# Kernel optimization log

Measured on AMD Instinct MI355X. Metric: run time of the kernel, lower is better.

Reference implementation:

```python
import jax, jax.numpy as jnp
import numpy as np

N_SITES = 64   # number of sampled indices (n = 2**6 in source)
CHI = 64       # virtual bond dimension of the isometric TN
BATCH = 32768  # number of independent perfect samples


def _isometrize(W):
    """Right-canonical isometrization (analog of mera.isometrize(method='cayley')).

    W: [n, chi, 2, chi] raw params -> A with sum_{s,r} A[l,s,r] A[l',s,r] = delta_{ll'}.
    """
    n, chi = W.shape[0], W.shape[1]
    M = W.reshape(n, chi, 2 * chi)               # [n, chi, 2*chi]
    Q, _ = jnp.linalg.qr(jnp.swapaxes(M, 1, 2))  # [n, 2*chi, chi], orthonormal columns
    return jnp.swapaxes(Q, 1, 2).reshape(n, chi, 2, chi)


def setup_inputs() -> dict:
    key = jax.random.key(0)
    k1, k2 = jax.random.split(key)
    W = jax.random.normal(k1, (N_SITES, CHI, 2, CHI), dtype=jnp.float32)
    u = jax.random.uniform(k2, (BATCH, N_SITES), dtype=jnp.float32)
    return {"W": W, "u": u}


def reference(W, u):
    """Perfect (autoregressive exact-conditional) sampling from an isometric TN.

    Returns:
      s_hat: [B, n, 2] one-hot samples, outcome 0 -> [0,1], outcome 1 -> [1,0]
             (matching v0=[0,1], v1=[1,0] in the source)
      prob:  [B, n] conditional probability of the drawn outcome at each step
             (the `probability` array the source maintains).
    """
    A = _isometrize(W)                 # [n, chi, 2, chi]
    B, n = u.shape
    chi = W.shape[1]
    # left boundary environment (unit norm) -> total norm is exactly 1
    L0 = jnp.zeros((B, chi), dtype=W.dtype).at[:, 0].set(1.0)

    def step(L, inp):
        A_i, u_i = inp                              # [chi,2,chi], [B]
        T = jnp.einsum('bl,lsr->bsr', L, A_i)       # [B, 2, chi]
        p = jnp.sum(T * T, axis=-1)                 # [B, 2]; p0 + p1 == 1 by isometry
        take1 = u_i >= p[:, 0]                      # r < ps0 -> outcome 0
        s = take1.astype(jnp.int32)
        p_s = jnp.where(take1, p[:, 1], p[:, 0])    # probability of chosen branch
        T_s = jnp.where(take1[:, None], T[:, 1, :], T[:, 0, :])
        L_new = T_s / jnp.sqrt(p_s)[:, None]        # renormalize by sqrt(prob)
        return L_new, (s, p_s)

    _, (s, p) = jax.lax.scan(step, L0, (A, u.T))    # s,p: [n, B]
    s = s.T                                         # [B, n]
    prob = p.T                                      # [B, n]
    s_hat = jax.nn.one_hot(1 - s, 2, dtype=W.dtype)  # 0 -> [0,1], 1 -> [1,0]
    return s_hat, prob
```

## Files before the change

kernel.cpp:

```cpp
#include <hip/hip_runtime.h>

#define NSITES 64
#define CHI 64
#define BATCH 32768
#define LPAD 66

typedef double d4 __attribute__((ext_vector_type(4)));

#define MFMA_HAZARD_FENCE() do {                                    \
    __builtin_amdgcn_sched_barrier(0);                              \
    asm volatile("s_nop 7\n\ts_nop 7\n\ts_nop 7\n\ts_nop 7" :::);   \
    __builtin_amdgcn_sched_barrier(0);                              \
} while (0)

__global__ __launch_bounds__(512) void qr_site_kernel(
    const float* __restrict__ W, double* __restrict__ A8)
{
    __shared__ double M[128][65];
    __shared__ double wpart[8][64];
    __shared__ double tauS[64];
    __shared__ double redS[2];
    __shared__ double vcol[136];

    const int i   = blockIdx.x;
    const int tid = threadIdx.x;

    for (int idx = tid; idx < 8192; idx += 512) {
        int l = idx >> 7, sr = idx & 127;
        M[sr][l] = (double)W[i * 8192 + idx];
    }
    __syncthreads();

    const int jf = tid & 63;
    const int gf = tid >> 6;
    const int r0 = gf * 16;

    for (int k = 0; k < 64; ++k) {
        const double alpha = M[k][k];
        double v2 = 0.0;
        if (tid < 128) { double xv = (tid > k) ? M[tid][k] : 0.0; v2 = xv * xv; }
        #pragma unroll
        for (int off = 32; off; off >>= 1) v2 += __shfl_down(v2, off, 64);
        if (tid < 128 && (tid & 63) == 0) redS[tid >> 6] = v2;
        __syncthreads();
        const double xnorm2 = redS[0] + redS[1];

        double beta, tk;
        if (xnorm2 == 0.0) { beta = alpha; tk = 0.0; }
        else {
            double nrm = sqrt(alpha * alpha + xnorm2);
            beta = (alpha >= 0.0) ? -nrm : nrm;
            tk   = (beta - alpha) / beta;
        }
        const double sc = (tk != 0.0) ? (1.0 / (alpha - beta)) : 0.0;
        if (tid < 128 && tid > k && tk != 0.0) M[tid][k] *= sc;
        if (tid == 0) tauS[k] = tk;
        __syncthreads();

        double part = 0.0;
        if (jf > k) {
            #pragma unroll 4
            for (int m = 0; m < 16; ++m) {
                int rr = r0 + m;
                double vr = (rr > k) ? M[rr][k] : ((rr == k) ? 1.0 : 0.0);
                part = fma(vr, M[rr][jf], part);
            }
        }
        wpart[gf][jf] = part;
        __syncthreads();
        if (jf > k) {
            double wj = tauS[k] * (wpart[0][jf] + wpart[1][jf] + wpart[2][jf] + wpart[3][jf]
                                 + wpart[4][jf] + wpart[5][jf] + wpart[6][jf] + wpart[7][jf]);
            #pragma unroll 4
            for (int m = 0; m < 16; ++m) {
                int rr = r0 + m;
                double vr = (rr > k) ? M[rr][k] : ((rr == k) ? 1.0 : 0.0);
                M[rr][jf] = fma(-vr, wj, M[rr][jf]);
            }
        }
        __syncthreads();
    }

    const int jq = tid >> 3;
    const int qq = tid & 7;
    double E[16];
    #pragma unroll
    for (int m = 0; m < 16; ++m) E[m] = ((qq * 16 + m) == jq) ? 1.0 : 0.0;

    for (int k = 63; k >= 0; --k) {
        if (tid < 128) {
            double val = (tid > k) ? M[tid][k] : ((tid == k) ? 1.0 : 0.0);
            vcol[tid + (tid >> 4)] = val;
        }
        __syncthreads();
        const double tk = tauS[k];
        double part = 0.0;
        #pragma unroll
        for (int m = 0; m < 16; ++m) {
            int rr = qq * 16 + m;
            part = fma(vcol[rr + qq], E[m], part);
        }
        part += __shfl_xor(part, 1, 64);
        part += __shfl_xor(part, 2, 64);
        part += __shfl_xor(part, 4, 64);
        const double wj = tk * part;
        #pragma unroll
        for (int m = 0; m < 16; ++m) {
            int rr = qq * 16 + m;
            E[m] = fma(-vcol[rr + qq], wj, E[m]);
        }
        __syncthreads();
    }

    double* dst = A8 + (size_t)i * 8192 + jq * 128 + qq * 16;
    #pragma unroll
    for (int m = 0; m < 16; ++m) dst[m] = E[m];
}

#define MFMA_ROW(bp, a)                                                   \
    c0 = __builtin_amdgcn_mfma_f64_16x16x4f64((a), (bp)[  0], c0, 0,0,0); \
    c1 = __builtin_amdgcn_mfma_f64_16x16x4f64((a), (bp)[ 16], c1, 0,0,0); \
    c2 = __builtin_amdgcn_mfma_f64_16x16x4f64((a), (bp)[ 32], c2, 0,0,0); \
    c3 = __builtin_amdgcn_mfma_f64_16x16x4f64((a), (bp)[ 48], c3, 0,0,0); \
    c4 = __builtin_amdgcn_mfma_f64_16x16x4f64((a), (bp)[ 64], c4, 0,0,0); \
    c5 = __builtin_amdgcn_mfma_f64_16x16x4f64((a), (bp)[ 80], c5, 0,0,0); \
    c6 = __builtin_amdgcn_mfma_f64_16x16x4f64((a), (bp)[ 96], c6, 0,0,0); \
    c7 = __builtin_amdgcn_mfma_f64_16x16x4f64((a), (bp)[112], c7, 0,0,0);

__global__ __launch_bounds__(512, 2) void sample_kernel(
    const double* __restrict__ A8, const float* __restrict__ u,
    float* __restrict__ out)
{
    __shared__ __align__(16) double As[8192];
    __shared__ double Lsm[128 * LPAD];

    const int tid  = threadIdx.x;
    const int w    = tid >> 6;
    const int lane = tid & 63;
    const int g    = lane >> 4;
    const int r    = lane & 15;
    const int ubase = blockIdx.x * 128 + 16 * w;

    d4 zp = {0.0, 0.0, 0.0, 0.0};
    const d4 rowP = __builtin_amdgcn_mfma_f64_16x16x4f64((g == 0) ? (double)r : 0.0, 1.0, zp, 0, 0, 0);
    const d4 colP = __builtin_amdgcn_mfma_f64_16x16x4f64((g == 0) ? 1.0 : 0.0, (double)r, zp, 0, 0, 0);
    MFMA_HAZARD_FENCE();
    const int row0 = (int)(rowP.x + 0.5), row1 = (int)(rowP.y + 0.5);
    const int row2 = (int)(rowP.z + 0.5), row3 = (int)(rowP.w + 0.5);
    const int col0 = (int)(colP.x + 0.5), col1 = (int)(colP.y + 0.5);
    const int col2 = (int)(colP.z + 0.5), col3 = (int)(colP.w + 0.5);

    for (int j = g; j < 64; j += 4)
        Lsm[(16 * w + r) * LPAD + j] = (j == 0) ? 1.0 : 0.0;

    {
        const double2* s2 = (const double2*)A8;
        double2* a2 = (double2*)As;
        #pragma unroll
        for (int q = 0; q < 8; ++q) a2[q * 512 + tid] = s2[q * 512 + tid];
    }
    __syncthreads();

    float* probOut = out + (size_t)BATCH * (NSITES * 2);

    for (int site = 0; site < NSITES; ++site) {
        const float u0 = u[(size_t)(ubase + row0) * NSITES + site];
        const float u1 = u[(size_t)(ubase + row1) * NSITES + site];
        const float u2 = u[(size_t)(ubase + row2) * NSITES + site];
        const float u3 = u[(size_t)(ubase + row3) * NSITES + site];

        d4 c0 = {0.0, 0.0, 0.0, 0.0}, c1 = c0, c2 = c0, c3 = c0;
        d4 c4 = c0, c5 = c0, c6 = c0, c7 = c0;

        const double* Lp = Lsm + (16 * w + r) * LPAD + g;
        const double* Ap = As + g * 128 + r;

        #pragma unroll
        for (int kk = 0; kk < 8; ++kk) {
            const double a = Lp[4 * kk];
            const double* bp = Ap + kk * 512;
            MFMA_ROW(bp, a)
        }

        double2 st0, st1, st2, st3;
        if (site < NSITES - 1) {
            const double2* nx = (const double2*)(A8 + (size_t)(site + 1) * 8192);
            st0 = nx[0 * 512 + tid]; st1 = nx[1 * 512 + tid];
            st2 = nx[2 * 512 + tid]; st3 = nx[3 * 512 + tid];
        }

        #pragma unroll
        for (int kk = 8; kk < 16; ++kk) {
            const double a = Lp[4 * kk];
            const double* bp = Ap + kk * 512;
            MFMA_ROW(bp, a)
        }

        __syncthreads();

        double2 st4, st5, st6, st7;
        if (site < NSITES - 1) {
            double2* a2 = (double2*)As;
            a2[0 * 512 + tid] = st0; a2[1 * 512 + tid] = st1;
            a2[2 * 512 + tid] = st2; a2[3 * 512 + tid] = st3;
            const double2* nx = (const double2*)(A8 + (size_t)(site + 1) * 8192);
            st4 = nx[4 * 512 + tid]; st5 = nx[5 * 512 + tid];
            st6 = nx[6 * 512 + tid]; st7 = nx[7 * 512 + tid];
        }

        MFMA_HAZARD_FENCE();

        double P0 = fma(c3.x, c3.x, fma(c2.x, c2.x, fma(c1.x, c1.x, c0.x * c0.x)));
        double P1 = fma(c3.y, c3.y, fma(c2.y, c2.y, fma(c1.y, c1.y, c0.y * c0.y)));
        double P2 = fma(c3.z, c3.z, fma(c2.z, c2.z, fma(c1.z, c1.z, c0.z * c0.z)));
        double P3 = fma(c3.w, c3.w, fma(c2.w, c2.w, fma(c1.w, c1.w, c0.w * c0.w)));
        #pragma unroll
        for (int m = 1; m <= 8; m <<= 1) {
            P0 += __shfl_xor(P0, m, 64);
            P1 += __shfl_xor(P1, m, 64);
            P2 += __shfl_xor(P2, m, 64);
            P3 += __shfl_xor(P3, m, 64);
        }

        const bool t0 = ((double)u0 >= P0);
        const bool t1 = ((double)u1 >= P1);
        const bool t2 = ((double)u2 >= P2);
        const bool t3 = ((double)u3 >= P3);
        const double s0 = t0 ? (1.0 - P0) : P0;
        const double s1 = t1 ? (1.0 - P1) : P1;
        const double s2 = t2 ? (1.0 - P2) : P2;
        const double s3 = t3 ? (1.0 - P3) : P3;
        const double i0 = rsqrt(s0);
        const double i1 = rsqrt(s1);
        const double i2 = rsqrt(s2);
        const double i3 = rsqrt(s3);

        double* LwB = Lsm + (16 * w) * LPAD;
        LwB[row0 * LPAD +  0 + col0] = (t0 ? c4.x : c0.x) * i0;
        LwB[row0 * LPAD + 16 + col0] = (t0 ? c5.x : c1.x) * i0;
        LwB[row0 * LPAD + 32 + col0] = (t0 ? c6.x : c2.x) * i0;
        LwB[row0 * LPAD + 48 + col0] = (t0 ? c7.x : c3.x) * i0;
        LwB[row1 * LPAD +  0 + col1] = (t1 ? c4.y : c0.y) * i1;
        LwB[row1 * LPAD + 16 + col1] = (t1 ? c5.y : c1.y) * i1;
        LwB[row1 * LPAD + 32 + col1] = (t1 ? c6.y : c2.y) * i1;
        LwB[row1 * LPAD + 48 + col1] = (t1 ? c7.y : c3.y) * i1;
        LwB[row2 * LPAD +  0 + col2] = (t2 ? c4.z : c0.z) * i2;
        LwB[row2 * LPAD + 16 + col2] = (t2 ? c5.z : c1.z) * i2;
        LwB[row2 * LPAD + 32 + col2] = (t2 ? c6.z : c2.z) * i2;
        LwB[row2 * LPAD + 48 + col2] = (t2 ? c7.z : c3.z) * i2;
        LwB[row3 * LPAD +  0 + col3] = (t3 ? c4.w : c0.w) * i3;
        LwB[row3 * LPAD + 16 + col3] = (t3 ? c5.w : c1.w) * i3;
        LwB[row3 * LPAD + 32 + col3] = (t3 ? c6.w : c2.w) * i3;
        LwB[row3 * LPAD + 48 + col3] = (t3 ? c7.w : c3.w) * i3;

        if (r == 0) {
            probOut[(size_t)(ubase + row0) * NSITES + site] = (float)s0;
            probOut[(size_t)(ubase + row1) * NSITES + site] = (float)s1;
            probOut[(size_t)(ubase + row2) * NSITES + site] = (float)s2;
            probOut[(size_t)(ubase + row3) * NSITES + site] = (float)s3;
            *(float2*)(out + (size_t)(ubase + row0) * 128 + site * 2) = make_float2(t0 ? 1.f : 0.f, t0 ? 0.f : 1.f);
            *(float2*)(out + (size_t)(ubase + row1) * 128 + site * 2) = make_float2(t1 ? 1.f : 0.f, t1 ? 0.f : 1.f);
            *(float2*)(out + (size_t)(ubase + row2) * 128 + site * 2) = make_float2(t2 ? 1.f : 0.f, t2 ? 0.f : 1.f);
            *(float2*)(out + (size_t)(ubase + row3) * 128 + site * 2) = make_float2(t3 ? 1.f : 0.f, t3 ? 0.f : 1.f);
        }

        if (site < NSITES - 1) {
            double2* a2 = (double2*)As;
            a2[4 * 512 + tid] = st4; a2[5 * 512 + tid] = st5;
            a2[6 * 512 + tid] = st6; a2[7 * 512 + tid] = st7;
        }
        __syncthreads();
    }
}

extern "C" void kernel_launch(void* const* d_in, const int* in_sizes, int n_in,
                              void* d_out, int out_size, void* d_ws, size_t ws_size,
                              hipStream_t stream)
{
    const float* W = (const float*)d_in[0];
    const float* u = (const float*)d_in[1];
    float* out = (float*)d_out;
    double* A8 = (double*)d_ws;

    hipLaunchKernelGGL(qr_site_kernel, dim3(NSITES), dim3(512), 0, stream, W, A8);
    hipLaunchKernelGGL(sample_kernel, dim3(256), dim3(512), 0, stream, A8, u, out);
}
```

Baseline: 814.9 us.

## Cut barriers in Householder QR and reorder sample-kernel MFMA halves around prefetch stores

The QR kernel now computes each next column norm inside the trailing update, so one reduction barrier per step goes away. It applies unnormalized reflectors with a rescaled tau. All Householder vectors are staged into a transposed shared buffer once, which removes both barriers per step in the Q back-accumulation, at the cost of about 70KB more LDS. In the sampling kernel, the second half of the MFMA chain moves after the mid-site barrier and the first prefetch store. The end-of-site barrier moves before the final prefetch store, giving more overlap between global loads and matrix ops.

Result: slower. 925.0 us (+13.5%).

```diff
diff --git a/kernel.cpp b/kernel.cpp
--- a/kernel.cpp
+++ b/kernel.cpp
@@ -19,8 +19,8 @@
     __shared__ double M[128][65];
     __shared__ double wpart[8][64];
     __shared__ double tauS[64];
-    __shared__ double redS[2];
-    __shared__ double vcol[136];
+    __shared__ double redS2[8];
+    __shared__ double Vt[64][136];
 
     const int i   = blockIdx.x;
     const int tid = threadIdx.x;
@@ -29,57 +29,91 @@
         int l = idx >> 7, sr = idx & 127;
         M[sr][l] = (double)W[i * 8192 + idx];
     }
-    __syncthreads();
 
     const int jf = tid & 63;
     const int gf = tid >> 6;
     const int r0 = gf * 16;
+    __syncthreads();
+
+    if (jf == 0) {
+        double s = 0.0;
+        #pragma unroll 4
+        for (int m = 0; m < 16; ++m) {
+            int rr = r0 + m;
+            double x = (rr >= 1) ? M[rr][0] : 0.0;
+            s = fma(x, x, s);
+        }
+        redS2[gf] = s;
+    }
+    __syncthreads();
 
     for (int k = 0; k < 64; ++k) {
+        const double v2 = ((redS2[0] + redS2[1]) + (redS2[2] + redS2[3]))
+                        + ((redS2[4] + redS2[5]) + (redS2[6] + redS2[7]));
         const double alpha = M[k][k];
-        double v2 = 0.0;
-        if (tid < 128) { double xv = (tid > k) ? M[tid][k] : 0.0; v2 = xv * xv; }
-        #pragma unroll
-        for (int off = 32; off; off >>= 1) v2 += __shfl_down(v2, off, 64);
-        if (tid < 128 && (tid & 63) == 0) redS[tid >> 6] = v2;
-        __syncthreads();
-        const double xnorm2 = redS[0] + redS[1];
-
         double beta, tk;
-        if (xnorm2 == 0.0) { beta = alpha; tk = 0.0; }
+        if (v2 == 0.0) { beta = alpha; tk = 0.0; }
         else {
-            double nrm = sqrt(alpha * alpha + xnorm2);
+            double nrm = sqrt(alpha * alpha + v2);
             beta = (alpha >= 0.0) ? -nrm : nrm;
             tk   = (beta - alpha) / beta;
         }
-        const double sc = (tk != 0.0) ? (1.0 / (alpha - beta)) : 0.0;
-        if (tid < 128 && tid > k && tk != 0.0) M[tid][k] *= sc;
+        const double uk   = alpha - beta;
+        const double sc   = (tk != 0.0) ? (1.0 / uk) : 0.0;
+        const double tau2 = (tk != 0.0) ? (tk / (uk * uk)) : 0.0;
         if (tid == 0) tauS[k] = tk;
-        __syncthreads();
-
+
+        double ureg[16];
+        #pragma unroll 4
+        for (int m = 0; m < 16; ++m) {
+            int rr = r0 + m;
+            ureg[m] = (rr > k) ? M[rr][k] : ((rr == k) ? uk : 0.0);
+        }
         double part = 0.0;
         if (jf > k) {
             #pragma unroll 4
-            for (int m = 0; m < 16; ++m) {
-                int rr = r0 + m;
-                double vr = (rr > k) ? M[rr][k] : ((rr == k) ? 1.0 : 0.0);
-                part = fma(vr, M[rr][jf], part);
-            }
+            for (int m = 0; m < 16; ++m)
+                part = fma(ureg[m], M[r0 + m][jf], part);
         }
         wpart[gf][jf] = part;
         __syncthreads();
+
         if (jf > k) {
-            double wj = tauS[k] * (wpart[0][jf] + wpart[1][jf] + wpart[2][jf] + wpart[3][jf]
-                                 + wpart[4][jf] + wpart[5][jf] + wpart[6][jf] + wpart[7][jf]);
+            double wj = tau2 * (((wpart[0][jf] + wpart[1][jf]) + (wpart[2][jf] + wpart[3][jf]))
+                              + ((wpart[4][jf] + wpart[5][jf]) + (wpart[6][jf] + wpart[7][jf])));
+            if (jf == k + 1) {
+                double s = 0.0;
+                #pragma unroll 4
+                for (int m = 0; m < 16; ++m) {
+                    int rr = r0 + m;
+                    double nv = fma(-ureg[m], wj, M[rr][jf]);
+                    M[rr][jf] = nv;
+                    if (rr > k + 1) s = fma(nv, nv, s);
+                }
+                redS2[gf] = s;
+            } else {
+                #pragma unroll 4
+                for (int m = 0; m < 16; ++m) {
+                    int rr = r0 + m;
+                    M[rr][jf] = fma(-ureg[m], wj, M[rr][jf]);
+                }
+            }
+        } else if (jf == k) {
             #pragma unroll 4
             for (int m = 0; m < 16; ++m) {
                 int rr = r0 + m;
-                double vr = (rr > k) ? M[rr][k] : ((rr == k) ? 1.0 : 0.0);
-                M[rr][jf] = fma(-vr, wj, M[rr][jf]);
+                if (rr > k) M[rr][k] = ureg[m] * sc;
             }
         }
         __syncthreads();
     }
+
+    for (int idx = tid; idx < 8192; idx += 512) {
+        int rr = idx & 127, k = idx >> 7;
+        double val = (rr > k) ? M[rr][k] : ((rr == k) ? 1.0 : 0.0);
+        Vt[k][rr + (rr >> 4)] = val;
+    }
+    __syncthreads();
 
     const int jq = tid >> 3;
     const int qq = tid & 7;
@@ -88,28 +122,22 @@
     for (int m = 0; m < 16; ++m) E[m] = ((qq * 16 + m) == jq) ? 1.0 : 0.0;
 
     for (int k = 63; k >= 0; --k) {
-        if (tid < 128) {
-            double val = (tid > k) ? M[tid][k] : ((tid == k) ? 1.0 : 0.0);
-            vcol[tid + (tid >> 4)] = val;
-        }
-        __syncthreads();
-        const double tk = tauS[k];
+        const double tkk = tauS[k];
         double part = 0.0;
         #pragma unroll
         for (int m = 0; m < 16; ++m) {
             int rr = qq * 16 + m;
-            part = fma(vcol[rr + qq], E[m], part);
+            part = fma(Vt[k][rr + qq], E[m], part);
         }
         part += __shfl_xor(part, 1, 64);
         part += __shfl_xor(part, 2, 64);
         part += __shfl_xor(part, 4, 64);
-        const double wj = tk * part;
+        const double wj = tkk * part;
         #pragma unroll
         for (int m = 0; m < 16; ++m) {
             int rr = qq * 16 + m;
-            E[m] = fma(-vcol[rr + qq], wj, E[m]);
-        }
-        __syncthreads();
+            E[m] = fma(-Vt[k][rr + qq], wj, E[m]);
+        }
     }
 
     double* dst = A8 + (size_t)i * 8192 + jq * 128 + qq * 16;
@@ -169,19 +197,6 @@
         const float u2 = u[(size_t)(ubase + row2) * NSITES + site];
         const float u3 = u[(size_t)(ubase + row3) * NSITES + site];
 
-        d4 c0 = {0.0, 0.0, 0.0, 0.0}, c1 = c0, c2 = c0, c3 = c0;
-        d4 c4 = c0, c5 = c0, c6 = c0, c7 = c0;
-
-        const double* Lp = Lsm + (16 * w + r) * LPAD + g;
-        const double* Ap = As + g * 128 + r;
-
-        #pragma unroll
-        for (int kk = 0; kk < 8; ++kk) {
-            const double a = Lp[4 * kk];
-            const double* bp = Ap + kk * 512;
-            MFMA_ROW(bp, a)
-        }
-
         double2 st0, st1, st2, st3;
         if (site < NSITES - 1) {
             const double2* nx = (const double2*)(A8 + (size_t)(site + 1) * 8192);
@@ -189,8 +204,14 @@
             st2 = nx[2 * 512 + tid]; st3 = nx[3 * 512 + tid];
         }
 
-        #pragma unroll
-        for (int kk = 8; kk < 16; ++kk) {
+        d4 c0 = {0.0, 0.0, 0.0, 0.0}, c1 = c0, c2 = c0, c3 = c0;
+        d4 c4 = c0, c5 = c0, c6 = c0, c7 = c0;
+
+        const double* Lp = Lsm + (16 * w + r) * LPAD + g;
+        const double* Ap = As + g * 128 + r;
+
+        #pragma unroll
+        for (int kk = 0; kk < 8; ++kk) {
             const double a = Lp[4 * kk];
             const double* bp = Ap + kk * 512;
             MFMA_ROW(bp, a)
@@ -208,6 +229,12 @@
             st6 = nx[6 * 512 + tid]; st7 = nx[7 * 512 + tid];
         }
 
+        #pragma unroll
+        for (int kk = 8; kk < 16; ++kk) {
+            const double a = Lp[4 * kk];
+            const double* bp = Ap + kk * 512;
+            MFMA_ROW(bp, a)
+        }
         MFMA_HAZARD_FENCE();
 
         double P0 = fma(c3.x, c3.x, fma(c2.x, c2.x, fma(c1.x, c1.x, c0.x * c0.x)));
@@ -264,12 +291,13 @@
             *(float2*)(out + (size_t)(ubase + row3) * 128 + site * 2) = make_float2(t3 ? 1.f : 0.f, t3 ? 0.f : 1.f);
         }
 
+        __syncthreads();
+
         if (site < NSITES - 1) {
             double2* a2 = (double2*)As;
             a2[4 * 512 + tid] = st4; a2[5 * 512 + tid] = st5;
             a2[6 * 512 + tid] = st6; a2[7 * 512 + tid] = st7;
         }
-        __syncthreads();
     }
 }
 
```
